# Performance work log

Measured on AMD Instinct MI355X. Metric: run time of the kernel, lower is better.

The kernel has to match this reference:

```python
import jax, jax.numpy as jnp
import numpy as np

STATE_DIM = 32
HIDDEN = 128
DT = 0.01


def _lstm_cell(inp, h, c, W, b):
    # inp: [B, D_in], h/c: [B, H], W: [D_in+H, 4H], b: [4H]
    gates = jnp.concatenate([inp, h], axis=-1) @ W + b
    i, f, g, o = jnp.split(gates, 4, axis=-1)
    i = jax.nn.sigmoid(i)
    f = jax.nn.sigmoid(f)
    g = jnp.tanh(g)
    o = jax.nn.sigmoid(o)
    c_new = f * c + i * g
    h_new = o * jnp.tanh(c_new)
    return h_new, c_new


def setup_inputs() -> dict:
    key = jax.random.key(0)
    ks = jax.random.split(key, 8)
    B = 8192
    s = lambda fan_in: 1.0 / np.sqrt(fan_in)
    W0 = jax.random.uniform(ks[0], (STATE_DIM + HIDDEN, 4 * HIDDEN), jnp.float32, -s(STATE_DIM + HIDDEN), s(STATE_DIM + HIDDEN))
    b0 = jax.random.uniform(ks[1], (4 * HIDDEN,), jnp.float32, -s(STATE_DIM + HIDDEN), s(STATE_DIM + HIDDEN))
    W1 = jax.random.uniform(ks[2], (HIDDEN + HIDDEN, 4 * HIDDEN), jnp.float32, -s(2 * HIDDEN), s(2 * HIDDEN))
    b1 = jax.random.uniform(ks[3], (4 * HIDDEN,), jnp.float32, -s(2 * HIDDEN), s(2 * HIDDEN))
    Wout = jax.random.uniform(ks[4], (HIDDEN, STATE_DIM), jnp.float32, -s(HIDDEN), s(HIDDEN))
    bout = jax.random.uniform(ks[5], (STATE_DIM,), jnp.float32, -s(HIDDEN), s(HIDDEN))
    dt_scale = jnp.ones((STATE_DIM,), jnp.float32) * 0.01
    x0 = jax.random.normal(ks[6], (B, STATE_DIM), jnp.float32)
    return {"x0": x0, "W0": W0, "b0": b0, "W1": W1, "b1": b1,
            "Wout": Wout, "bout": bout, "dt_scale": dt_scale, "num_steps": 512}


def reference(x0, W0, b0, W1, b1, Wout, bout, dt_scale, num_steps):
    B = x0.shape[0]
    h0 = jnp.zeros((B, HIDDEN), x0.dtype)
    c0 = jnp.zeros((B, HIDDEN), x0.dtype)

    def step(carry, _):
        x, h0_, c0_, h1_, c1_ = carry
        h0n, c0n = _lstm_cell(x, h0_, c0_, W0, b0)
        h1n, c1n = _lstm_cell(h0n, h1_, c1_, W1, b1)
        dx_dt = h1n @ Wout + bout
        x_new = x + dx_dt * dt_scale * DT
        return (x_new, h0n, c0n, h1n, c1n), x_new

    _, xs = jax.lax.scan(step, (x0, h0, c0, h0, c0), None, length=num_steps)
    # xs: [T, B, D] -> trajectory [B, T+1, D]
    traj = jnp.concatenate([x0[:, None, :], jnp.transpose(xs, (1, 0, 2))], axis=1)
    return traj
```

## Files before the change

### kernel.cpp

```cpp
#include <hip/hip_runtime.h>
#include <hip/hip_bf16.h>

typedef __bf16  bf16x8  __attribute__((ext_vector_type(8)));
typedef short   short8_t __attribute__((ext_vector_type(8)));
typedef float   float4_t __attribute__((ext_vector_type(4)));

#define MFMA(a, b, c) __builtin_amdgcn_mfma_f32_16x16x32_bf16((a), (b), (c), 0, 0, 0)

#define LOG2E      1.4426950408889634f
#define TWO_LOG2E  2.8853900817779268f

__device__ __forceinline__ unsigned short f2bf(float f) {
  unsigned u = __builtin_bit_cast(unsigned, f);
  unsigned r = ((u >> 16) & 1u) + 0x7FFFu;
  return (unsigned short)((u + r) >> 16);
}
__device__ __forceinline__ float sig2(float x) {
  return __builtin_amdgcn_rcpf(1.f + __builtin_amdgcn_exp2f(-x));
}
__device__ __forceinline__ float tanh2s(float x) {
  return 1.f - 2.f * __builtin_amdgcn_rcpf(1.f + __builtin_amdgcn_exp2f(x));
}

__global__ __launch_bounds__(512, 2) void lstm_roll(
    const float* __restrict__ x0,  const float* __restrict__ W0,
    const float* __restrict__ b0v, const float* __restrict__ W1,
    const float* __restrict__ b1v, const float* __restrict__ Wout,
    const float* __restrict__ bout, const float* __restrict__ dts,
    const int* __restrict__ nsp,   float* __restrict__ out)
{
  __shared__ __align__(16) unsigned short w0h[8 * 4 * 4 * 512];
  __shared__ __align__(16) unsigned short woutF[2 * 4 * 512];
  __shared__ __align__(16) unsigned short h0f0[4 * 512];
  __shared__ __align__(16) unsigned short h0f1[4 * 512];
  __shared__ __align__(16) unsigned short h1f0[4 * 512];
  __shared__ __align__(16) unsigned short h1f1[4 * 512];
  __shared__ __align__(16) unsigned short xf0[512];
  __shared__ __align__(16) unsigned short xf1[512];

  const int tid = threadIdx.x;
  const int w   = tid >> 6;
  const int l   = tid & 63;
  const int lm  = l & 15;
  const int lh  = l >> 4;
  const int T   = nsp[0];
  const long rowStride = (long)(T + 1) * 32;
  const long bbase = (long)blockIdx.x * 32;

  bf16x8 w0x[4];
  bf16x8 w1f[4][8];
  #pragma unroll
  for (int g = 0; g < 4; ++g) {
    const float sc = (g == 2) ? TWO_LOG2E : LOG2E;
    const int col = g * 128 + w * 16 + lm;
    {
      short8_t t8;
      #pragma unroll
      for (int e = 0; e < 8; ++e) t8[e] = (short)f2bf(sc * W0[(lh * 8 + e) * 512 + col]);
      w0x[g] = __builtin_bit_cast(bf16x8, t8);
    }
    #pragma unroll
    for (int kt = 0; kt < 8; ++kt) {
      short8_t t8;
      #pragma unroll
      for (int e = 0; e < 8; ++e) t8[e] = (short)f2bf(sc * W1[(kt * 32 + lh * 8 + e) * 512 + col]);
      w1f[g][kt] = __builtin_bit_cast(bf16x8, t8);
    }
    #pragma unroll
    for (int kt = 0; kt < 4; ++kt) {
      const int base = (((w * 4 + g) * 4) + kt) * 512 + l * 8;
      #pragma unroll
      for (int e = 0; e < 8; ++e)
        w0h[base + e] = f2bf(sc * W0[(32 + kt * 32 + lh * 8 + e) * 512 + col]);
    }
  }
  {
    const int n = w & 1, kt = w >> 1;
    if (kt < 4) {
      const float csc = dts[n * 16 + lm] * 0.01f;
      const int base = (n * 4 + kt) * 512 + l * 8;
      #pragma unroll
      for (int e = 0; e < 8; ++e)
        woutF[base + e] = f2bf(csc * Wout[(kt * 32 + lh * 8 + e) * 32 + (n * 16 + lm)]);
    }
  }
  float b0r[4], b1r[4];
  #pragma unroll
  for (int g = 0; g < 4; ++g) {
    const float sc = (g == 2) ? TWO_LOG2E : LOG2E;
    b0r[g] = sc * b0v[g * 128 + w * 16 + lm];
    b1r[g] = sc * b1v[g * 128 + w * 16 + lm];
  }

  const int S_w = (w >> 1) & 1;
  const int n_c = w & 1;
  float boutr = 0.f, xr[4] = {0.f, 0.f, 0.f, 0.f};
  long obase0 = 0;
  int  xfb = 0;
  if (w < 4) {
    boutr = bout[n_c * 16 + lm] * dts[n_c * 16 + lm] * 0.01f;
    const int kin = n_c * 16 + lm;
    xfb = (lh * 4 + 16 * (kin >> 3)) * 8 + (kin & 7);
    obase0 = (bbase + S_w * 16 + lh * 4) * rowStride + (n_c * 16 + lm);
    unsigned short* xfS = S_w ? xf1 : xf0;
    #pragma unroll
    for (int r = 0; r < 4; ++r) {
      xr[r] = x0[(bbase + S_w * 16 + lh * 4 + r) * 32 + n_c * 16 + lm];
      out[obase0 + r * rowStride] = xr[r];
      xfS[xfb + r * 8] = f2bf(xr[r]);
    }
  }
  for (int i = tid; i < 4 * 512; i += 512) {
    h0f0[i] = 0; h0f1[i] = 0; h1f0[i] = 0; h1f1[i] = 0;
  }

  const int hwb = (w >> 1) * 512 +
                  (lh * 4 + 16 * (2 * (w & 1) + ((lm >> 3) & 1))) * 8 + (lm & 7);

  float4_t c0s0 = {0.f,0.f,0.f,0.f}, c0s1 = {0.f,0.f,0.f,0.f};
  float4_t c1s0 = {0.f,0.f,0.f,0.f}, c1s1 = {0.f,0.f,0.f,0.f};

#define INIT4(ACC, B) \
    _Pragma("unroll") \
    for (int g = 0; g < 4; ++g) (ACC)[g] = (float4_t){(B)[g], (B)[g], (B)[g], (B)[g]};

#define CELL0H(HSRC, ACC) \
    _Pragma("unroll") \
    for (int kt = 0; kt < 4; ++kt) { \
      const bf16x8 a = *(const bf16x8*)&(HSRC)[kt * 512 + l * 8]; \
      _Pragma("unroll") \
      for (int g = 0; g < 4; ++g) { \
        const bf16x8 bw = *(const bf16x8*)&w0h[(((w * 4 + g) * 4) + kt) * 512 + l * 8]; \
        (ACC)[g] = MFMA(a, bw, (ACC)[g]); \
      } \
    }

#define XPART(XSRC, ACC) { \
    const bf16x8 ax = *(const bf16x8*)&(XSRC)[l * 8]; \
    _Pragma("unroll") \
    for (int g = 0; g < 4; ++g) (ACC)[g] = MFMA(ax, w0x[g], (ACC)[g]); \
  }

#define CELL1A(H0SRC, AM) \
    _Pragma("unroll") \
    for (int kt = 0; kt < 4; ++kt) { \
      const bf16x8 a = *(const bf16x8*)&(H0SRC)[kt * 512 + l * 8]; \
      _Pragma("unroll") \
      for (int g = 0; g < 4; ++g) (AM)[g] = MFMA(a, w1f[g][kt], (AM)[g]); \
    }
#define CELL1B(H1SRC, AM) \
    _Pragma("unroll") \
    for (int kt = 0; kt < 4; ++kt) { \
      const bf16x8 a = *(const bf16x8*)&(H1SRC)[kt * 512 + l * 8]; \
      _Pragma("unroll") \
      for (int g = 0; g < 4; ++g) (AM)[g] = MFMA(a, w1f[g][kt + 4], (AM)[g]); \
    }

#define ACT4(ACC, CS, DST) \
    _Pragma("unroll") \
    for (int r = 0; r < 4; ++r) { \
      const float iv = sig2((ACC)[0][r]); \
      const float fv = sig2((ACC)[1][r]); \
      const float gv = tanh2s((ACC)[2][r]); \
      const float ov = sig2((ACC)[3][r]); \
      const float cc = fv * (CS)[r] + iv * gv; \
      (CS)[r] = cc; \
      const float hv = ov * tanh2s(cc * TWO_LOG2E); \
      DST; \
    }

#define PROJ(H1SRC, XFDST) { \
    float4_t dacc = (float4_t){boutr, boutr, boutr, boutr}; \
    _Pragma("unroll") \
    for (int kt = 0; kt < 4; ++kt) { \
      const bf16x8 a  = *(const bf16x8*)&(H1SRC)[kt * 512 + l * 8]; \
      const bf16x8 bw = *(const bf16x8*)&woutF[(n_c * 4 + kt) * 512 + l * 8]; \
      dacc = MFMA(a, bw, dacc); \
    } \
    _Pragma("unroll") \
    for (int r = 0; r < 4; ++r) { \
      xr[r] += dacc[r]; \
      (XFDST)[xfb + r * 8] = f2bf(xr[r]); \
    } \
  }

  float4_t am1[4];
  INIT4(am1, b1r);

  __syncthreads();

  #pragma unroll 1
  for (int t = 0; t < T; ++t) {
    float4_t acc0s0[4];
    INIT4(acc0s0, b0r);
    CELL0H(h0f0, acc0s0);
    if (t > 0) {
      ACT4(am1, c1s1, h1f1[hwb + r * 8] = f2bf(hv));
      if (w < 2) PROJ(h1f0, xf0);
    }
    __syncthreads();

    float4_t acc0s1[4];
    XPART(xf0, acc0s0);
    INIT4(acc0s1, b0r);
    CELL0H(h0f1, acc0s1);
    ACT4(acc0s0, c0s0, h0f0[hwb + r * 8] = f2bf(hv));
    if (w >= 2 && w < 4 && t > 0) PROJ(h1f1, xf1);
    __syncthreads();

    if (w < 2 && t > 0) {
      const long ob = obase0 + (long)t * 32;
      #pragma unroll
      for (int r = 0; r < 4; ++r) out[ob + r * rowStride] = xr[r];
    }
    float4_t am0[4];
    INIT4(am0, b1r);
    CELL1A(h0f0, am0);
    XPART(xf1, acc0s1);
    ACT4(acc0s1, c0s1, h0f1[hwb + r * 8] = f2bf(hv));
    CELL1B(h1f0, am0);
    __syncthreads();

    if (w >= 2 && w < 4 && t > 0) {
      const long ob = obase0 + (long)t * 32;
      #pragma unroll
      for (int r = 0; r < 4; ++r) out[ob + r * rowStride] = xr[r];
    }
    ACT4(am0, c1s0, h1f0[hwb + r * 8] = f2bf(hv));
    INIT4(am1, b1r);
    CELL1A(h0f1, am1);
    CELL1B(h1f1, am1);
    __syncthreads();
  }

  ACT4(am1, c1s1, h1f1[hwb + r * 8] = f2bf(hv));
  if (w < 2) {
    float4_t dacc = (float4_t){boutr, boutr, boutr, boutr};
    #pragma unroll
    for (int kt = 0; kt < 4; ++kt) {
      const bf16x8 a  = *(const bf16x8*)&h1f0[kt * 512 + l * 8];
      const bf16x8 bw = *(const bf16x8*)&woutF[(n_c * 4 + kt) * 512 + l * 8];
      dacc = MFMA(a, bw, dacc);
    }
    const long ob = obase0 + (long)T * 32;
    #pragma unroll
    for (int r = 0; r < 4; ++r) {
      xr[r] += dacc[r];
      out[ob + r * rowStride] = xr[r];
    }
  }
  __syncthreads();
  if (w >= 2 && w < 4) {
    float4_t dacc = (float4_t){boutr, boutr, boutr, boutr};
    #pragma unroll
    for (int kt = 0; kt < 4; ++kt) {
      const bf16x8 a  = *(const bf16x8*)&h1f1[kt * 512 + l * 8];
      const bf16x8 bw = *(const bf16x8*)&woutF[(n_c * 4 + kt) * 512 + l * 8];
      dacc = MFMA(a, bw, dacc);
    }
    const long ob = obase0 + (long)T * 32;
    #pragma unroll
    for (int r = 0; r < 4; ++r) {
      xr[r] += dacc[r];
      out[ob + r * rowStride] = xr[r];
    }
  }
}

extern "C" void kernel_launch(void* const* d_in, const int* in_sizes, int n_in,
                              void* d_out, int out_size, void* d_ws, size_t ws_size,
                              hipStream_t stream) {
  (void)n_in; (void)out_size; (void)d_ws; (void)ws_size;
  const float* x0   = (const float*)d_in[0];
  const float* W0   = (const float*)d_in[1];
  const float* b0   = (const float*)d_in[2];
  const float* W1   = (const float*)d_in[3];
  const float* b1   = (const float*)d_in[4];
  const float* Wout = (const float*)d_in[5];
  const float* bout = (const float*)d_in[6];
  const float* dts  = (const float*)d_in[7];
  const int*   nsp  = (const int*)d_in[8];
  float* out = (float*)d_out;

  const int B    = in_sizes[0] / 32;
  const int grid = B / 32;
  lstm_roll<<<dim3(grid), dim3(512), 0, stream>>>(x0, W0, b0, W1, b1, Wout, bout, dts, nsp, out);
}
```

Measured before the change: 2.280 ms.

## Interleave MFMA with activations, lighten barriers and activation math

Reorders each sub-step so the independent MFMA chains (cell-1 B part, next-cell accumulations, output projection) are issued before the activation math that would otherwise stall on them, letting matrix work overlap with transcendental ALU work. Replaces __syncthreads with an LDS-only waitcnt plus s_barrier, which avoids waiting on outstanding global stores. Folds constants into the tanh/gate algebra to save a few multiplies, and uses the hardware bf16 conversion instead of manual rounding. The main risks are higher register pressure from values kept live longer, and the barrier being correct only if no global memory ordering is needed across it.

```diff
diff --git a/kernel.cpp b/kernel.cpp
--- a/kernel.cpp
+++ b/kernel.cpp
@@ -10,16 +10,16 @@
 #define LOG2E      1.4426950408889634f
 #define TWO_LOG2E  2.8853900817779268f
 
+#define BAR() do {                                            \
+    asm volatile("s_waitcnt lgkmcnt(0)" ::: "memory");        \
+    __builtin_amdgcn_s_barrier();                             \
+  } while (0)
+
 __device__ __forceinline__ unsigned short f2bf(float f) {
-  unsigned u = __builtin_bit_cast(unsigned, f);
-  unsigned r = ((u >> 16) & 1u) + 0x7FFFu;
-  return (unsigned short)((u + r) >> 16);
+  return __builtin_bit_cast(unsigned short, static_cast<__bf16>(f));
 }
 __device__ __forceinline__ float sig2(float x) {
   return __builtin_amdgcn_rcpf(1.f + __builtin_amdgcn_exp2f(-x));
-}
-__device__ __forceinline__ float tanh2s(float x) {
-  return 1.f - 2.f * __builtin_amdgcn_rcpf(1.f + __builtin_amdgcn_exp2f(x));
 }
 
 __global__ __launch_bounds__(512, 2) void lstm_roll(
@@ -161,25 +161,29 @@
     for (int r = 0; r < 4; ++r) { \
       const float iv = sig2((ACC)[0][r]); \
       const float fv = sig2((ACC)[1][r]); \
-      const float gv = tanh2s((ACC)[2][r]); \
+      const float tg = __builtin_amdgcn_rcpf(1.f + __builtin_amdgcn_exp2f((ACC)[2][r])); \
       const float ov = sig2((ACC)[3][r]); \
-      const float cc = fv * (CS)[r] + iv * gv; \
+      const float gs = TWO_LOG2E - 2.f * TWO_LOG2E * tg; \
+      const float cc = fv * (CS)[r] + iv * gs; \
       (CS)[r] = cc; \
-      const float hv = ov * tanh2s(cc * TWO_LOG2E); \
+      const float tc = __builtin_amdgcn_rcpf(1.f + __builtin_amdgcn_exp2f(cc)); \
+      const float hv = ov - 2.f * ov * tc; \
       DST; \
     }
 
-#define PROJ(H1SRC, XFDST) { \
-    float4_t dacc = (float4_t){boutr, boutr, boutr, boutr}; \
+#define PROJ_MFMA(H1SRC, DACC) { \
+    DACC = (float4_t){boutr, boutr, boutr, boutr}; \
     _Pragma("unroll") \
     for (int kt = 0; kt < 4; ++kt) { \
       const bf16x8 a  = *(const bf16x8*)&(H1SRC)[kt * 512 + l * 8]; \
       const bf16x8 bw = *(const bf16x8*)&woutF[(n_c * 4 + kt) * 512 + l * 8]; \
-      dacc = MFMA(a, bw, dacc); \
+      DACC = MFMA(a, bw, DACC); \
     } \
+  }
+#define PROJ_FIN(XFDST, DACC) { \
     _Pragma("unroll") \
     for (int r = 0; r < 4; ++r) { \
-      xr[r] += dacc[r]; \
+      xr[r] += DACC[r]; \
       (XFDST)[xfb + r * 8] = f2bf(xr[r]); \
     } \
   }
@@ -187,7 +191,7 @@
   float4_t am1[4];
   INIT4(am1, b1r);
 
-  __syncthreads();
+  BAR();
 
   #pragma unroll 1
   for (int t = 0; t < T; ++t) {
@@ -195,18 +199,25 @@
     INIT4(acc0s0, b0r);
     CELL0H(h0f0, acc0s0);
     if (t > 0) {
+      float4_t dacc;
+      if (w < 2) PROJ_MFMA(h1f0, dacc);
       ACT4(am1, c1s1, h1f1[hwb + r * 8] = f2bf(hv));
-      if (w < 2) PROJ(h1f0, xf0);
-    }
-    __syncthreads();
+      if (w < 2) PROJ_FIN(xf0, dacc);
+    }
+    BAR();
 
     float4_t acc0s1[4];
     XPART(xf0, acc0s0);
     INIT4(acc0s1, b0r);
     CELL0H(h0f1, acc0s1);
-    ACT4(acc0s0, c0s0, h0f0[hwb + r * 8] = f2bf(hv));
-    if (w >= 2 && w < 4 && t > 0) PROJ(h1f1, xf1);
-    __syncthreads();
+    {
+      float4_t dacc;
+      const bool pw = (w >= 2 && w < 4 && t > 0);
+      if (pw) PROJ_MFMA(h1f1, dacc);
+      ACT4(acc0s0, c0s0, h0f0[hwb + r * 8] = f2bf(hv));
+      if (pw) PROJ_FIN(xf1, dacc);
+    }
+    BAR();
 
     if (w < 2 && t > 0) {
       const long ob = obase0 + (long)t * 32;
@@ -217,31 +228,26 @@
     INIT4(am0, b1r);
     CELL1A(h0f0, am0);
     XPART(xf1, acc0s1);
+    CELL1B(h1f0, am0);
     ACT4(acc0s1, c0s1, h0f1[hwb + r * 8] = f2bf(hv));
-    CELL1B(h1f0, am0);
-    __syncthreads();
+    BAR();
 
     if (w >= 2 && w < 4 && t > 0) {
       const long ob = obase0 + (long)t * 32;
       #pragma unroll
       for (int r = 0; r < 4; ++r) out[ob + r * rowStride] = xr[r];
     }
-    ACT4(am0, c1s0, h1f0[hwb + r * 8] = f2bf(hv));
     INIT4(am1, b1r);
     CELL1A(h0f1, am1);
     CELL1B(h1f1, am1);
-    __syncthreads();
+    ACT4(am0, c1s0, h1f0[hwb + r * 8] = f2bf(hv));
+    BAR();
   }
 
   ACT4(am1, c1s1, h1f1[hwb + r * 8] = f2bf(hv));
   if (w < 2) {
-    float4_t dacc = (float4_t){boutr, boutr, boutr, boutr};
-    #pragma unroll
-    for (int kt = 0; kt < 4; ++kt) {
-      const bf16x8 a  = *(const bf16x8*)&h1f0[kt * 512 + l * 8];
-      const bf16x8 bw = *(const bf16x8*)&woutF[(n_c * 4 + kt) * 512 + l * 8];
-      dacc = MFMA(a, bw, dacc);
-    }
+    float4_t dacc;
+    PROJ_MFMA(h1f0, dacc);
     const long ob = obase0 + (long)T * 32;
     #pragma unroll
     for (int r = 0; r < 4; ++r) {
@@ -249,15 +255,10 @@
       out[ob + r * rowStride] = xr[r];
     }
   }
-  __syncthreads();
+  BAR();
   if (w >= 2 && w < 4) {
-    float4_t dacc = (float4_t){boutr, boutr, boutr, boutr};
-    #pragma unroll
-    for (int kt = 0; kt < 4; ++kt) {
-      const bf16x8 a  = *(const bf16x8*)&h1f1[kt * 512 + l * 8];
-      const bf16x8 bw = *(const bf16x8*)&woutF[(n_c * 4 + kt) * 512 + l * 8];
-      dacc = MFMA(a, bw, dacc);
-    }
+    float4_t dacc;
+    PROJ_MFMA(h1f1, dacc);
     const long ob = obase0 + (long)T * 32;
     #pragma unroll
     for (int r = 0; r < 4; ++r) {
```

Measured after the change: 2.817 ms. +23.5%, slower.
